# Kernel tuning notes

Hardware: AMD Instinct MI355X
Metric: run time of the kernel (lower is better)

Reference implementation:

```python
import jax, jax.numpy as jnp
import numpy as np

MAX_WAVELENGTH = 10000
BIG_NEG = -2.3819763e38

def _rope(x, positions):
    # x: [B, L, H, D], positions: [B, L] float32
    d = x.shape[-1]
    freq_exp = 2.0 / d * jnp.arange(d // 2, dtype=jnp.float32)
    timescale = MAX_WAVELENGTH ** freq_exp
    radians = (positions[..., None] / timescale[None, None, :])[..., None, :]  # [B,L,1,D/2]
    sin, cos = jnp.sin(radians), jnp.cos(radians)
    x1, x2 = jnp.split(x, 2, axis=-1)
    return jnp.concatenate([x1 * cos - x2 * sin, x2 * cos + x1 * sin], axis=-1).astype(x.dtype)

def _adaln_rmsnorm(x, cond, Wmod, bmod):
    # RMSNorm in fp32, then AdaLN scale/shift; returns (normed, gate[B,1,D])
    var = jnp.mean(jnp.square(x.astype(jnp.float32)), axis=-1, keepdims=True)
    normed = x * jax.lax.rsqrt(var + 1e-6)
    mod = (cond @ Wmod + bmod)[:, None, :]  # [B,1,3D]
    scale, shift, gate = jnp.split(mod, 3, axis=-1)
    return (normed * (1 + scale) + shift).astype(x.dtype), gate

def setup_inputs() -> dict:
    key = jax.random.key(0)
    ks = jax.random.split(key, 9)
    B, T, D, F, N, K, H = 2, 2048, 2048, 16384, 8, 1, 256
    x = jax.random.normal(ks[0], (B, T, D), jnp.float32)
    positions = jnp.broadcast_to(jnp.arange(T, dtype=jnp.float32), (B, T))
    attn_mask = jnp.broadcast_to(jnp.tril(jnp.ones((T, T), dtype=bool))[None, None], (B, 1, T, T))
    cond = jax.random.normal(ks[1], (B, D), jnp.float32)
    Wmod_a = jax.random.normal(ks[2], (D, 3 * D), jnp.float32) * 0.02
    bmod_a = jnp.zeros((3 * D,), jnp.float32)
    Wq = jax.random.normal(ks[3], (N, D, H), jnp.float32) * (D ** -0.5)
    Wkv = jax.random.normal(ks[4], (2, K, D, H), jnp.float32) * (D ** -0.5)
    Wo = jax.random.normal(ks[5], (N, H, D), jnp.float32) * ((N * H) ** -0.5)
    Wmod_f = jax.random.normal(ks[6], (D, 3 * D), jnp.float32) * 0.02
    bmod_f = jnp.zeros((3 * D,), jnp.float32)
    Wg = jax.random.normal(ks[7], (2, D, F), jnp.float32) * (D ** -0.5)
    Wl = jax.random.normal(ks[8], (F, D), jnp.float32) * (F ** -0.5)
    return dict(x=x, positions=positions, attn_mask=attn_mask, cond=cond,
                Wmod_a=Wmod_a, bmod_a=bmod_a, Wq=Wq, Wkv=Wkv, Wo=Wo,
                Wmod_f=Wmod_f, bmod_f=bmod_f, Wg=Wg, Wl=Wl)

def reference(x, positions, attn_mask, cond, Wmod_a, bmod_a, Wq, Wkv, Wo, Wmod_f, bmod_f, Wg, Wl):
    K = Wkv.shape[1]               # num_kv_heads
    H = Wq.shape[-1]               # head_dim
    # --- pre-attention AdaLN RMSNorm ---
    n, gate_a = _adaln_rmsnorm(x, cond, Wmod_a, bmod_a)
    # --- GQA projections ---
    q = jnp.einsum('BTD,NDH->BTNH', n, Wq)
    k = jnp.einsum('BSD,KDH->BSKH', n, Wkv[0])
    v = jnp.einsum('BSD,KDH->BSKH', n, Wkv[1])
    q = _rope(q, positions) * (H ** -0.5)
    k = _rope(k, positions)
    B, T, N, _ = q.shape
    q = q.reshape(B, T, K, N // K, H)  # B T K G H
    logits = jnp.einsum('BTKGH,BSKH->BKGTS', q, k, preferred_element_type=jnp.float32)
    masked = jnp.where(attn_mask[:, :, None, :, :], logits, BIG_NEG)
    probs = jax.nn.softmax(masked, axis=-1).astype(x.dtype)
    enc = jnp.einsum('BKGTS,BSKH->BTKGH', probs, v).reshape(B, T, N, H)
    attn_out = jnp.einsum('BTNH,NHD->BTD', enc, Wo)
    # gated residual
    x = x + attn_out * gate_a
    # --- pre-FFN AdaLN RMSNorm + gated-GeLU MLP ---
    n, gate_f = _adaln_rmsnorm(x, cond, Wmod_f, bmod_f)
    h = jax.nn.gelu(jnp.einsum('BTD,DF->BTF', n, Wg[0])) * jnp.einsum('BTD,DF->BTF', n, Wg[1])
    mlp_out = jnp.einsum('BTF,FD->BTD', h, Wl)
    return x + mlp_out * gate_f
```

## Files before the change

### kernel.cpp

```cpp
#include <hip/hip_runtime.h>
#include <hip/hip_bf16.h>

typedef __bf16 bf16_t;
typedef __bf16 bf16x8 __attribute__((ext_vector_type(8)));
typedef float  f32x4  __attribute__((ext_vector_type(4)));

#define DEV static __device__ __forceinline__

DEV void gload16(const bf16_t* g, bf16_t* l) {
    __builtin_amdgcn_global_load_lds(
        (const __attribute__((address_space(1))) void*)g,
        (__attribute__((address_space(3))) void*)l, 16, 0, 0);
}

enum { EPI_F32 = 0, EPI_BF16 = 1, EPI_RES = 2, EPI_GELU = 3, EPI_MUL = 4 };

#define MFMA16(QQ, AR, BR)                                                    \
  _Pragma("unroll")                                                           \
  for (int nj = 0; nj < 4; nj++) {                                            \
    acc[(QQ)*4+0][nj] = __builtin_amdgcn_mfma_f32_16x16x32_bf16(AR[0], BR[nj], acc[(QQ)*4+0][nj], 0, 0, 0); \
    acc[(QQ)*4+1][nj] = __builtin_amdgcn_mfma_f32_16x16x32_bf16(AR[1], BR[nj], acc[(QQ)*4+1][nj], 0, 0, 0); \
    acc[(QQ)*4+2][nj] = __builtin_amdgcn_mfma_f32_16x16x32_bf16(AR[2], BR[nj], acc[(QQ)*4+2][nj], 0, 0, 0); \
    acc[(QQ)*4+3][nj] = __builtin_amdgcn_mfma_f32_16x16x32_bf16(AR[3], BR[nj], acc[(QQ)*4+3][nj], 0, 0, 0); \
  }

#define READA(BUF, QQ, CI, AR)                                                \
  _Pragma("unroll")                                                           \
  for (int mi = 0; mi < 4; mi++)                                              \
    AR[mi] = *(const bf16x8*)(rbA##BUF##CI + (QQ) * 4096 + mi * 1024);

#define READB(BUF, CI, BR)                                                    \
  _Pragma("unroll")                                                           \
  for (int nj = 0; nj < 4; nj++)                                              \
    BR[nj] = *(const bf16x8*)(rbB##BUF##CI + nj * 1024);

#define PHASE(RD_STMT, QQ, AR, BR, STAGE_STMT, WAIT_STMT)                     \
  { RD_STMT STAGE_STMT                                                        \
    __builtin_amdgcn_s_barrier();                                             \
    asm volatile("s_waitcnt lgkmcnt(0)" ::: "memory");                        \
    __builtin_amdgcn_sched_barrier(0);                                        \
    __builtin_amdgcn_s_setprio(1);                                            \
    MFMA16(QQ, AR, BR);                                                       \
    __builtin_amdgcn_s_setprio(0);                                            \
    WAIT_STMT                                                                 \
    __builtin_amdgcn_s_barrier(); }

template<int EPI>
__global__ __launch_bounds__(512, 1)
void gemm8p(const bf16_t* __restrict__ A, const bf16_t* __restrict__ Bt,
            void* __restrict__ Cout, int Kd, int lda, int ldb, int ldc,
            long sCz,
            const float* __restrict__ res, const float* __restrict__ gate,
            int gateStride, int rowsPerB, const bf16_t* __restrict__ aux)
{
    const int nbx = gridDim.x;
    const int nwg = nbx * gridDim.y;
    int lin = blockIdx.y * nbx + blockIdx.x;
    const int q8 = nwg >> 3, r8 = nwg & 7;
    const int xcd = lin & 7, oo = lin >> 3;
    lin = (xcd < r8 ? xcd * (q8 + 1) : r8 * (q8 + 1) + (xcd - r8) * q8) + oo;
    const long m0 = (long)(lin / nbx) * 256;
    const long n0 = (long)(lin % nbx) * 256;
    const long kb = (long)blockIdx.z * Kd;

    const int tid = threadIdx.x;
    const int l   = tid & 63;
    const int w   = tid >> 6;
    const int wr  = w >> 2;
    const int wcn = w & 3;

    __shared__ bf16_t sA[2][16384];
    __shared__ bf16_t sB[2][16384];

    const long sgc = (long)(((l & 7) ^ (l >> 3)) << 3);
    const int NT = Kd >> 6;
    const int NI = NT >> 1;

    const bf16_t* pA0 = A + (m0 + 0 * 64 + w * 8 + (l >> 3)) * (long)lda + kb + sgc;
    const bf16_t* pA1 = A + (m0 + 1 * 64 + w * 8 + (l >> 3)) * (long)lda + kb + sgc;
    const bf16_t* pA2 = A + (m0 + 2 * 64 + w * 8 + (l >> 3)) * (long)lda + kb + sgc;
    const bf16_t* pA3 = A + (m0 + 3 * 64 + w * 8 + (l >> 3)) * (long)lda + kb + sgc;
    const bf16_t* pB0 = Bt + (n0 + 0 * 64 + w * 8 + (l >> 3)) * (long)ldb + kb + sgc;
    const bf16_t* pB1 = Bt + (n0 + 1 * 64 + w * 8 + (l >> 3)) * (long)ldb + kb + sgc;
    const bf16_t* pB2 = Bt + (n0 + 2 * 64 + w * 8 + (l >> 3)) * (long)ldb + kb + sgc;
    const bf16_t* pB3 = Bt + (n0 + 3 * 64 + w * 8 + (l >> 3)) * (long)ldb + kb + sgc;

#define SCA(kt, bi, c) gload16(pA##c + (kt), &sA[bi][(c) * 4096 + w * 512])
#define SCB(kt, bi, c) gload16(pB##c + (kt), &sB[bi][(c) * 4096 + w * 512])

    f32x4 acc[8][4];
#pragma unroll
    for (int i = 0; i < 8; i++)
#pragma unroll
        for (int j = 0; j < 4; j++) acc[i][j] = f32x4{0.f, 0.f, 0.f, 0.f};

    const int co0 = ((l >> 4) ^ (l & 7)) << 3;
    const int co1 = ((4 + (l >> 4)) ^ (l & 7)) << 3;

    const bf16_t* rbA00 = &sA[0][(wr * 128 + (l & 15)) * 64 + co0];
    const bf16_t* rbA01 = &sA[0][(wr * 128 + (l & 15)) * 64 + co1];
    const bf16_t* rbA10 = &sA[1][(wr * 128 + (l & 15)) * 64 + co0];
    const bf16_t* rbA11 = &sA[1][(wr * 128 + (l & 15)) * 64 + co1];
    const bf16_t* rbB00 = &sB[0][(wcn * 64 + (l & 15)) * 64 + co0];
    const bf16_t* rbB01 = &sB[0][(wcn * 64 + (l & 15)) * 64 + co1];
    const bf16_t* rbB10 = &sB[1][(wcn * 64 + (l & 15)) * 64 + co0];
    const bf16_t* rbB11 = &sB[1][(wcn * 64 + (l & 15)) * 64 + co1];

    SCA(0, 0, 0); SCA(0, 0, 1); SCA(0, 0, 2); SCA(0, 0, 3);
    SCB(0, 0, 0); SCB(0, 0, 1); SCB(0, 0, 2); SCB(0, 0, 3);
    SCA(64, 1, 0); SCA(64, 1, 2); SCB(64, 1, 0); SCB(64, 1, 1);
    asm volatile("s_waitcnt vmcnt(4)" ::: "memory");
    __builtin_amdgcn_s_barrier();

    bf16x8 b0[4], b1[4], aR[4];

    for (int it = 0; it < NI; ++it) {
        const long kv  = (long)(2 * it + 1) * 64;
        const long kc  = (long)(2 * it + 2) * 64;
        const long kd2 = (long)(2 * it + 3) * 64;
        const bool hc  = (2 * it + 2) < NT;

        PHASE({ READB(0, 0, b0); READA(0, 0, 0, aR); }, 0, aR, b0,
              { SCB(kv, 1, 2); SCB(kv, 1, 3); }, {})
        PHASE({ READB(0, 1, b1); READA(0, 0, 1, aR); }, 0, aR, b1,
              { SCA(kv, 1, 1); SCA(kv, 1, 3); }, {})
        PHASE({ READA(0, 1, 0, aR); }, 1, aR, b0,
              { if (hc) { SCA(kc, 0, 0); SCA(kc, 0, 2); } }, {})
        PHASE({ READA(0, 1, 1, aR); }, 1, aR, b1,
              { if (hc) { SCB(kc, 0, 0); SCB(kc, 0, 1); } },
              { if (hc) { asm volatile("s_waitcnt vmcnt(4)" ::: "memory"); }
                else    { asm volatile("s_waitcnt vmcnt(0)" ::: "memory"); } })
        PHASE({ READB(1, 0, b0); READA(1, 0, 0, aR); }, 0, aR, b0,
              { if (hc) { SCB(kc, 0, 2); SCB(kc, 0, 3); } }, {})
        PHASE({ READB(1, 1, b1); READA(1, 0, 1, aR); }, 0, aR, b1,
              { if (hc) { SCA(kc, 0, 1); SCA(kc, 0, 3); } }, {})
        PHASE({ READA(1, 1, 0, aR); }, 1, aR, b0,
              { if (hc) { SCA(kd2, 1, 0); SCA(kd2, 1, 2); } }, {})
        PHASE({ READA(1, 1, 1, aR); }, 1, aR, b1,
              { if (hc) { SCB(kd2, 1, 0); SCB(kd2, 1, 1); } },
              { if (hc) { asm volatile("s_waitcnt vmcnt(4)" ::: "memory"); }
                else    { asm volatile("s_waitcnt vmcnt(0)" ::: "memory"); } })
    }

#pragma unroll
    for (int mi = 0; mi < 8; mi++) {
#pragma unroll
        for (int nj = 0; nj < 4; nj++) {
            f32x4 v = acc[mi][nj];
            const long col   = n0 + wcn * 64 + nj * 16 + (l & 15);
            const long row0r = m0 + wr * 128 + mi * 16 + ((l >> 4) * 4);
#pragma unroll
            for (int e = 0; e < 4; e++) {
                const long row = row0r + e;
                const long idx = row * (long)ldc + col + (long)blockIdx.z * sCz;
                const float val = v[e];
                if constexpr (EPI == EPI_F32) {
                    ((float*)Cout)[idx] = val;
                } else if constexpr (EPI == EPI_BF16) {
                    ((bf16_t*)Cout)[idx] = (bf16_t)val;
                } else if constexpr (EPI == EPI_RES) {
                    const int b = (int)(row / rowsPerB);
                    ((float*)Cout)[idx] = res[row * (long)ldc + col] + val * gate[(long)b * gateStride + col];
                } else if constexpr (EPI == EPI_GELU) {
                    const float gl = 0.5f * val * (1.f + tanhf(0.7978845608f * (val + 0.044715f * val * val * val)));
                    ((bf16_t*)Cout)[idx] = (bf16_t)gl;
                } else if constexpr (EPI == EPI_MUL) {
                    ((bf16_t*)Cout)[idx] = (bf16_t)((float)aux[idx] * val);
                }
            }
        }
    }
#undef SCA
#undef SCB
}

__global__ __launch_bounds__(256)
void combine_splitk(const float* __restrict__ P, const float* __restrict__ X1,
                    const float* __restrict__ gate, float* __restrict__ out,
                    int D, int T, int gateStride, long zstride, long n4)
{
    for (long i4 = (long)blockIdx.x * 256 + threadIdx.x; i4 < n4; i4 += (long)gridDim.x * 256) {
        const long i = i4 * 4;
        const float4 p0 = *(const float4*)(P + i);
        const float4 p1 = *(const float4*)(P + i + zstride);
        const float4 xv = *(const float4*)(X1 + i);
        const long row = i / D;
        const int  b   = (int)(row / T);
        const int  col = (int)(i - row * D);
        const float* gp = gate + (long)b * gateStride + col;
        float4 r;
        r.x = xv.x + (p0.x + p1.x) * gp[0];
        r.y = xv.y + (p0.y + p1.y) * gp[1];
        r.z = xv.z + (p0.z + p1.z) * gp[2];
        r.w = xv.w + (p0.w + p1.w) * gp[3];
        *(float4*)(out + i) = r;
    }
}

template<int EPI, int CAUSAL>
__global__ __launch_bounds__(256)
void gemm_bt(const bf16_t* __restrict__ A, const bf16_t* __restrict__ Bt,
             void* __restrict__ Cout,
             int M, int N, int Kd, int lda, int ldb, int ldc,
             long sAz, long sBz, long sCz,
             const float* __restrict__ res, const float* __restrict__ gate,
             int gateStride, int rowsPerB, const bf16_t* __restrict__ aux)
{
    const int tid = threadIdx.x;
    const int l   = tid & 63;
    const int w   = tid >> 6;
    const int wr  = w >> 1, wc = w & 1;
    const long m0 = (long)blockIdx.y * 128;
    const long n0 = (long)blockIdx.x * 128;
    const int  z  = blockIdx.z;

    if constexpr (CAUSAL == 1) {
        if (n0 > m0 + 127) return;
    }
    int kend = Kd;
    if constexpr (CAUSAL == 2) {
        const int kc = (int)m0 + 128;
        kend = kc < Kd ? kc : Kd;
    }

    A  += (long)z * sAz;
    Bt += (long)z * sBz;

    __shared__ bf16_t As[128 * 32];
    __shared__ bf16_t Bs[128 * 32];

    const int srow = w * 16 + (l >> 2);
    const int scol = (l & 3) * 8;
    const bf16_t* Ag = A  + (m0 + srow) * (long)lda + scol;
    const bf16_t* Bg = Bt + (n0 + srow) * (long)ldb + scol;

    bf16_t* ldsA = As + w * 512;
    bf16_t* ldsB = Bs + w * 512;

    f32x4 acc[16];
    const f32x4 fz = {0.f, 0.f, 0.f, 0.f};
#pragma unroll
    for (int i = 0; i < 16; i++) acc[i] = fz;

    for (int k0 = 0; k0 < kend; k0 += 32) {
        gload16(Ag + k0,                  ldsA);
        gload16(Ag + k0 + 64 * (long)lda, ldsA + 2048);
        gload16(Bg + k0,                  ldsB);
        gload16(Bg + k0 + 64 * (long)ldb, ldsB + 2048);
        __syncthreads();

        bf16x8 af[4], bfr[4];
#pragma unroll
        for (int f = 0; f < 4; f++) {
            af[f]  = *(const bf16x8*)(As + (wr * 64 + f * 16 + (l & 15)) * 32 + (l >> 4) * 8);
            bfr[f] = *(const bf16x8*)(Bs + (wc * 64 + f * 16 + (l & 15)) * 32 + (l >> 4) * 8);
        }
#pragma unroll
        for (int i = 0; i < 4; i++)
#pragma unroll
            for (int j = 0; j < 4; j++)
                acc[i * 4 + j] = __builtin_amdgcn_mfma_f32_16x16x32_bf16(af[i], bfr[j], acc[i * 4 + j], 0, 0, 0);
        __syncthreads();
    }

#pragma unroll
    for (int i = 0; i < 4; i++) {
#pragma unroll
        for (int j = 0; j < 4; j++) {
            f32x4 v = acc[i * 4 + j];
            const long col  = n0 + wc * 64 + j * 16 + (l & 15);
            const long row0 = m0 + wr * 64 + i * 16 + ((l >> 4) * 4);
#pragma unroll
            for (int e = 0; e < 4; e++) {
                const long row = row0 + e;
                const long idx = row * (long)ldc + col + (long)z * sCz;
                const float val = v[e];
                if constexpr (EPI == EPI_F32) {
                    ((float*)Cout)[idx] = val;
                } else if constexpr (EPI == EPI_BF16) {
                    ((bf16_t*)Cout)[idx] = (bf16_t)val;
                } else if constexpr (EPI == EPI_RES) {
                    const int b = (int)(row / rowsPerB);
                    ((float*)Cout)[idx] = res[row * (long)ldc + col] + val * gate[(long)b * gateStride + col];
                } else if constexpr (EPI == EPI_GELU) {
                    const float gl = 0.5f * val * (1.f + tanhf(0.7978845608f * (val + 0.044715f * val * val * val)));
                    ((bf16_t*)Cout)[idx] = (bf16_t)gl;
                } else {
                    ((bf16_t*)Cout)[idx] = (bf16_t)((float)aux[idx] * val);
                }
            }
        }
    }
}

__global__ __launch_bounds__(256)
void transpose_f2b(const float* __restrict__ in, bf16_t* __restrict__ out,
                   int R, int C, long inStride, long outStride)
{
    __shared__ float tile[32][33];
    in  += (long)blockIdx.z * inStride;
    out += (long)blockIdx.z * outStride;
    const int c0 = blockIdx.x * 32, r0 = blockIdx.y * 32;
    const int tx = threadIdx.x, ty = threadIdx.y;
#pragma unroll
    for (int i = 0; i < 4; i++)
        tile[ty + i * 8][tx] = in[(long)(r0 + ty + i * 8) * C + c0 + tx];
    __syncthreads();
#pragma unroll
    for (int i = 0; i < 4; i++)
        out[(long)(c0 + ty + i * 8) * R + r0 + tx] = (bf16_t)tile[tx][ty + i * 8];
}

__global__ __launch_bounds__(256)
void modk_part(const float* __restrict__ cond, const float* __restrict__ W,
               float* __restrict__ part, int D3, int KS)
{
    const int j = blockIdx.x * 256 + threadIdx.x;
    const int b = blockIdx.y;
    const int z = blockIdx.z;
    const float* cb = cond + (long)b * (KS * gridDim.z);
    float s = 0.f;
    const int d0 = z * KS;
#pragma unroll 4
    for (int d = d0; d < d0 + KS; d++) s += cb[d] * W[(long)d * D3 + j];
    part[((long)z * gridDim.y + b) * D3 + j] = s;
}

__global__ __launch_bounds__(256)
void modk_reduce(const float* __restrict__ part, const float* __restrict__ bvec,
                 float* __restrict__ mod, int D3, int NZ)
{
    const int j = blockIdx.x * 256 + threadIdx.x;
    const int b = blockIdx.y;
    float s = bvec[j];
    for (int z = 0; z < NZ; z++) s += part[((long)z * gridDim.y + b) * D3 + j];
    mod[(long)b * D3 + j] = s;
}

__global__ __launch_bounds__(256)
void rmsnorm_adaln(const float* __restrict__ xin, const float* __restrict__ mod,
                   bf16_t* __restrict__ out, int D, int T, int D3)
{
    const long row = blockIdx.x;
    const int  b   = (int)(row / T);
    const int  tid = threadIdx.x;
    const float4* x4 = (const float4*)(xin + row * (long)D);
    const float4 v0 = x4[tid], v1 = x4[tid + 256];
    float ss = v0.x * v0.x + v0.y * v0.y + v0.z * v0.z + v0.w * v0.w
             + v1.x * v1.x + v1.y * v1.y + v1.z * v1.z + v1.w * v1.w;
    for (int o = 32; o; o >>= 1) ss += __shfl_down(ss, o, 64);
    __shared__ float red[4];
    if ((tid & 63) == 0) red[tid >> 6] = ss;
    __syncthreads();
    ss = red[0] + red[1] + red[2] + red[3];
    const float rs = rsqrtf(ss / (float)D + 1e-6f);
    const float* sc = mod + (long)b * D3;
    const float* sh = sc + D;
    const float4 s0 = ((const float4*)sc)[tid], s1 = ((const float4*)sc)[tid + 256];
    const float4 h0 = ((const float4*)sh)[tid], h1 = ((const float4*)sh)[tid + 256];
    bf16_t* orow = out + row * (long)D;
    orow[tid * 4 + 0]         = (bf16_t)(v0.x * rs * (1.f + s0.x) + h0.x);
    orow[tid * 4 + 1]         = (bf16_t)(v0.y * rs * (1.f + s0.y) + h0.y);
    orow[tid * 4 + 2]         = (bf16_t)(v0.z * rs * (1.f + s0.z) + h0.z);
    orow[tid * 4 + 3]         = (bf16_t)(v0.w * rs * (1.f + s0.w) + h0.w);
    orow[(tid + 256) * 4 + 0] = (bf16_t)(v1.x * rs * (1.f + s1.x) + h1.x);
    orow[(tid + 256) * 4 + 1] = (bf16_t)(v1.y * rs * (1.f + s1.y) + h1.y);
    orow[(tid + 256) * 4 + 2] = (bf16_t)(v1.z * rs * (1.f + s1.z) + h1.z);
    orow[(tid + 256) * 4 + 3] = (bf16_t)(v1.w * rs * (1.f + s1.w) + h1.w);
}

__global__ __launch_bounds__(128)
void rope_q(const bf16_t* __restrict__ qp, const float* __restrict__ positions,
            bf16_t* __restrict__ qo, int T, int ldq, int H)
{
    const int t = blockIdx.x, n = blockIdx.y, b = blockIdx.z;
    const int i = threadIdx.x;
    const long in0 = ((long)(b * T + t)) * ldq + n * H;
    const float x1 = (float)qp[in0 + i];
    const float x2 = (float)qp[in0 + i + 128];
    const float pos = positions[b * T + t];
    const float inv = expf(-9.210340371976184f * (float)i / 128.f);
    float s, c;
    sincosf(pos * inv, &s, &c);
    const float scl = 0.0625f;
    const long out0 = (((long)(b * 8 + n)) * T + t) * H;
    qo[out0 + i]       = (bf16_t)((x1 * c - x2 * s) * scl);
    qo[out0 + i + 128] = (bf16_t)((x2 * c + x1 * s) * scl);
}

__global__ __launch_bounds__(128)
void rope_kv(const bf16_t* __restrict__ kvp, const float* __restrict__ positions,
             bf16_t* __restrict__ ko, bf16_t* __restrict__ vt, int T, int H, int S, int ldkv)
{
    const int t = blockIdx.x, b = blockIdx.y;
    const int i = threadIdx.x;
    const long in0 = ((long)(b * T + t)) * ldkv;
    const float k1 = (float)kvp[in0 + i];
    const float k2 = (float)kvp[in0 + i + 128];
    const float pos = positions[b * T + t];
    const float inv = expf(-9.210340371976184f * (float)i / 128.f);
    float s, c;
    sincosf(pos * inv, &s, &c);
    const long ko0 = ((long)(b * T + t)) * H;
    ko[ko0 + i]       = (bf16_t)(k1 * c - k2 * s);
    ko[ko0 + i + 128] = (bf16_t)(k2 * c + k1 * s);
    vt[((long)b * H + i) * S + t]       = kvp[in0 + 256 + i];
    vt[((long)b * H + i + 128) * S + t] = kvp[in0 + 256 + i + 128];
}

__global__ __launch_bounds__(256)
void softmax_causal(const float* __restrict__ sc, bf16_t* __restrict__ pr, int T, int S)
{
    const int t = blockIdx.x, g = blockIdx.y;
    const long row = (long)g * T + t;
    const float* srow = sc + row * S;
    bf16_t* prow = pr + row * S;
    const int tid = threadIdx.x;
    const int limit = t | 127;
    const int nch = (limit >> 8) + 1;
    float vals[8];
    float mx = -3.4e38f;
    for (int i = 0; i < nch; i++) {
        const int s = i * 256 + tid;
        const float v = (s <= t) ? srow[s] : -3.4e38f;
        vals[i] = v;
        mx = fmaxf(mx, v);
    }
    for (int o = 32; o; o >>= 1) mx = fmaxf(mx, __shfl_down(mx, o, 64));
    __shared__ float red[4];
    if ((tid & 63) == 0) red[tid >> 6] = mx;
    __syncthreads();
    mx = fmaxf(fmaxf(red[0], red[1]), fmaxf(red[2], red[3]));
    __syncthreads();
    float sum = 0.f;
    for (int i = 0; i < nch; i++) {
        const int s = i * 256 + tid;
        const float e = (s <= t) ? __expf(vals[i] - mx) : 0.f;
        vals[i] = e;
        sum += e;
    }
    for (int o = 32; o; o >>= 1) sum += __shfl_down(sum, o, 64);
    if ((tid & 63) == 0) red[tid >> 6] = sum;
    __syncthreads();
    sum = red[0] + red[1] + red[2] + red[3];
    const float invs = 1.f / sum;
    for (int i = 0; i < nch; i++)
        prow[i * 256 + tid] = (bf16_t)(vals[i] * invs);
}

extern "C" void kernel_launch(void* const* d_in, const int* in_sizes, int n_in,
                              void* d_out, int out_size, void* d_ws, size_t ws_size,
                              hipStream_t stream)
{
    const float* x      = (const float*)d_in[0];
    const float* pos    = (const float*)d_in[1];
    const float* cond   = (const float*)d_in[3];
    const float* Wmod_a = (const float*)d_in[4];
    const float* bmod_a = (const float*)d_in[5];
    const float* Wq     = (const float*)d_in[6];
    const float* Wkv    = (const float*)d_in[7];
    const float* Wo     = (const float*)d_in[8];
    const float* Wmod_f = (const float*)d_in[9];
    const float* bmod_f = (const float*)d_in[10];
    const float* Wg     = (const float*)d_in[11];
    const float* Wl     = (const float*)d_in[12];

    constexpr int  Bb = 2, T = 2048, D = 2048, F = 16384, Nh = 8, H = 256;
    constexpr int  NH = 2048, S = 2048, G = 8, BT = 4096, D3 = 6144;
    constexpr int  KSLICE = 64, NZ = D / KSLICE;
    constexpr int  NQKV = 2560;

    char* ws = (char*)d_ws;
    size_t off = 0;
    auto alloc = [&](size_t bytes) { char* p = ws + off; off += bytes; return p; };

    bf16_t* WQT  = (bf16_t*)alloc((size_t)NH * D * 2);
    bf16_t* WKVT = (bf16_t*)alloc((size_t)512 * D * 2);
    bf16_t* WOT  = (bf16_t*)alloc((size_t)D * NH * 2);
    bf16_t* WGT  = (bf16_t*)alloc((size_t)2 * F * D * 2);
    bf16_t* WLT  = (bf16_t*)alloc((size_t)D * F * 2);
    float*  MODA = (float*)alloc((size_t)Bb * D3 * 4);
    float*  MODF = (float*)alloc((size_t)Bb * D3 * 4);
    float*  PART = (float*)alloc((size_t)NZ * Bb * D3 * 4);
    bf16_t* NA   = (bf16_t*)alloc((size_t)BT * D * 2);
    bf16_t* QKVP = (bf16_t*)alloc((size_t)BT * NQKV * 2);
    bf16_t* Qr   = (bf16_t*)alloc((size_t)Bb * Nh * T * H * 2);
    bf16_t* Kr   = (bf16_t*)alloc((size_t)Bb * T * H * 2);
    bf16_t* VT   = (bf16_t*)alloc((size_t)Bb * H * S * 2);
    bf16_t* ENC  = (bf16_t*)alloc((size_t)BT * NH * 2);
    float*  X1   = (float*)alloc((size_t)BT * D * 4);
    bf16_t* NF   = (bf16_t*)alloc((size_t)BT * D * 2);
    const size_t scBytes = (size_t)G * T * S * 4;
    const size_t prBytes = (size_t)G * T * S * 2;
    const size_t hBytes  = (size_t)BT * F * 2;
    const size_t bigBytes = (scBytes + prBytes > hBytes) ? (scBytes + prBytes) : hBytes;
    char* big = alloc(bigBytes);
    float*  SC = (float*)big;
    bf16_t* PR = (bf16_t*)(big + scBytes);
    bf16_t* Hb = (bf16_t*)big;
    float*  PARTK = (float*)(big + hBytes);
    (void)ws_size; (void)in_sizes; (void)n_in; (void)out_size;

    const dim3 tb(32, 8);
    transpose_f2b<<<dim3(H / 32, D / 32, 8), tb, 0, stream>>>(Wq,  WQT,  D,  H, (long)D * H, (long)H * D);
    transpose_f2b<<<dim3(H / 32, D / 32, 2), tb, 0, stream>>>(Wkv, WKVT, D,  H, (long)D * H, (long)H * D);
    transpose_f2b<<<dim3(D / 32, NH / 32, 1), tb, 0, stream>>>(Wo, WOT, NH,  D, 0, 0);
    transpose_f2b<<<dim3(F / 32, D / 32, 2), tb, 0, stream>>>(Wg,  WGT,  D,  F, (long)D * F, (long)F * D);
    transpose_f2b<<<dim3(D / 32, F / 32, 1), tb, 0, stream>>>(Wl,  WLT,  F,  D, 0, 0);
    modk_part<<<dim3(D3 / 256, Bb, NZ), 256, 0, stream>>>(cond, Wmod_a, PART, D3, KSLICE);
    modk_reduce<<<dim3(D3 / 256, Bb), 256, 0, stream>>>(PART, bmod_a, MODA, D3, NZ);
    modk_part<<<dim3(D3 / 256, Bb, NZ), 256, 0, stream>>>(cond, Wmod_f, PART, D3, KSLICE);
    modk_reduce<<<dim3(D3 / 256, Bb), 256, 0, stream>>>(PART, bmod_f, MODF, D3, NZ);
    rmsnorm_adaln<<<BT, 256, 0, stream>>>(x, MODA, NA, D, T, D3);
    gemm8p<EPI_BF16><<<dim3(NQKV / 256, BT / 256, 1), 512, 0, stream>>>(
        NA, WQT, QKVP, D, D, D, NQKV, 0, nullptr, nullptr, 0, 0, nullptr);
    rope_q<<<dim3(T, Nh, Bb), 128, 0, stream>>>(QKVP, pos, Qr, T, NQKV, H);
    rope_kv<<<dim3(T, Bb), 128, 0, stream>>>(QKVP + NH, pos, Kr, VT, T, H, S, NQKV);
    for (int b = 0; b < Bb; b++) {
        gemm_bt<EPI_F32, 1><<<dim3(S / 128, T / 128, G), 256, 0, stream>>>(
            Qr + (long)b * Nh * T * H, Kr + (long)b * T * H, SC,
            T, S, H, H, H, S, (long)T * H, 0, (long)T * S, nullptr, nullptr, 0, 0, nullptr);
        softmax_causal<<<dim3(T, G), 256, 0, stream>>>(SC, PR, T, S);
        gemm_bt<EPI_BF16, 2><<<dim3(H / 128, T / 128, G), 256, 0, stream>>>(
            PR, VT + (long)b * H * S, ENC + (long)b * T * NH,
            T, H, S, S, S, NH, (long)T * S, 0, (long)H, nullptr, nullptr, 0, 0, nullptr);
    }
    gemm8p<EPI_RES><<<dim3(D / 256, BT / 256, 1), 512, 0, stream>>>(
        ENC, WOT, X1, NH, NH, NH, D, 0, x, MODA + 2 * D, D3, T, nullptr);
    rmsnorm_adaln<<<BT, 256, 0, stream>>>(X1, MODF, NF, D, T, D3);
    gemm8p<EPI_GELU><<<dim3(F / 256, BT / 256, 1), 512, 0, stream>>>(
        NF, WGT, Hb, D, D, D, F, 0, nullptr, nullptr, 0, 0, nullptr);
    gemm8p<EPI_MUL><<<dim3(F / 256, BT / 256, 1), 512, 0, stream>>>(
        NF, WGT + (long)F * D, Hb, D, D, D, F, 0, nullptr, nullptr, 0, 0, Hb);
    gemm8p<EPI_F32><<<dim3(D / 256, BT / 256, 2), 512, 0, stream>>>(
        Hb, WLT, PARTK, F / 2, F, F, D, (long)BT * D, nullptr, nullptr, 0, 0, nullptr);
    combine_splitk<<<2048, 256, 0, stream>>>(
        PARTK, X1, MODF + 2 * D, (float*)d_out, D, T, D3, (long)BT * D, (long)BT * D / 4);
}
```

Before: 1.564 ms.

## Replace 8-phase ping-pong GEMM pipeline with simple double-buffered stage/compute loop

The main GEMM kernel drops its 8-phase interleaved schedule, which used split half-tile staging, setprio and sched barriers, in favour of a plainer double-buffered loop. Each iteration stages a full 64-wide K tile into the other buffer, waits, then runs all 32 MFMAs per sub-K chunk after loading 8 A and 4 B fragments at once. This cuts barrier count and scheduling complexity. It gives up the fine-grained overlap of LDS reads with MFMAs and the priority hints, and it raises register pressure from holding more fragments at once.

```diff
diff --git a/kernel.cpp b/kernel.cpp
--- a/kernel.cpp
+++ b/kernel.cpp
@@ -15,43 +15,37 @@
 
 enum { EPI_F32 = 0, EPI_BF16 = 1, EPI_RES = 2, EPI_GELU = 3, EPI_MUL = 4 };
 
-#define MFMA16(QQ, AR, BR)                                                    \
-  _Pragma("unroll")                                                           \
-  for (int nj = 0; nj < 4; nj++) {                                            \
-    acc[(QQ)*4+0][nj] = __builtin_amdgcn_mfma_f32_16x16x32_bf16(AR[0], BR[nj], acc[(QQ)*4+0][nj], 0, 0, 0); \
-    acc[(QQ)*4+1][nj] = __builtin_amdgcn_mfma_f32_16x16x32_bf16(AR[1], BR[nj], acc[(QQ)*4+1][nj], 0, 0, 0); \
-    acc[(QQ)*4+2][nj] = __builtin_amdgcn_mfma_f32_16x16x32_bf16(AR[2], BR[nj], acc[(QQ)*4+2][nj], 0, 0, 0); \
-    acc[(QQ)*4+3][nj] = __builtin_amdgcn_mfma_f32_16x16x32_bf16(AR[3], BR[nj], acc[(QQ)*4+3][nj], 0, 0, 0); \
+#define G_MFMA(d, a, b) d = __builtin_amdgcn_mfma_f32_16x16x32_bf16(a, b, d, 0, 0, 0)
+
+#define COMPUTE(AB0, AB1, BB0, BB1)                                           \
+  { bf16x8 aF[8], bF[4];                                                      \
+    _Pragma("unroll") for (int m8 = 0; m8 < 8; m8++)                          \
+      aF[m8] = *(const bf16x8*)(AB0 + (m8 >> 2) * 4096 + (m8 & 3) * 1024);    \
+    _Pragma("unroll") for (int nj = 0; nj < 4; nj++)                          \
+      bF[nj] = *(const bf16x8*)(BB0 + nj * 1024);                             \
+    _Pragma("unroll") for (int m8 = 0; m8 < 8; m8++)                          \
+      _Pragma("unroll") for (int nj = 0; nj < 4; nj++)                        \
+        G_MFMA(acc[m8][nj], aF[m8], bF[nj]);                                  \
+    _Pragma("unroll") for (int m8 = 0; m8 < 8; m8++)                          \
+      aF[m8] = *(const bf16x8*)(AB1 + (m8 >> 2) * 4096 + (m8 & 3) * 1024);    \
+    _Pragma("unroll") for (int nj = 0; nj < 4; nj++)                          \
+      bF[nj] = *(const bf16x8*)(BB1 + nj * 1024);                             \
+    _Pragma("unroll") for (int m8 = 0; m8 < 8; m8++)                          \
+      _Pragma("unroll") for (int nj = 0; nj < 4; nj++)                        \
+        G_MFMA(acc[m8][nj], aF[m8], bF[nj]);                                  \
   }
 
-#define READA(BUF, QQ, CI, AR)                                                \
-  _Pragma("unroll")                                                           \
-  for (int mi = 0; mi < 4; mi++)                                              \
-    AR[mi] = *(const bf16x8*)(rbA##BUF##CI + (QQ) * 4096 + mi * 1024);
-
-#define READB(BUF, CI, BR)                                                    \
-  _Pragma("unroll")                                                           \
-  for (int nj = 0; nj < 4; nj++)                                              \
-    BR[nj] = *(const bf16x8*)(rbB##BUF##CI + nj * 1024);
-
-#define PHASE(RD_STMT, QQ, AR, BR, STAGE_STMT, WAIT_STMT)                     \
-  { RD_STMT STAGE_STMT                                                        \
-    __builtin_amdgcn_s_barrier();                                             \
-    asm volatile("s_waitcnt lgkmcnt(0)" ::: "memory");                        \
-    __builtin_amdgcn_sched_barrier(0);                                        \
-    __builtin_amdgcn_s_setprio(1);                                            \
-    MFMA16(QQ, AR, BR);                                                       \
-    __builtin_amdgcn_s_setprio(0);                                            \
-    WAIT_STMT                                                                 \
-    __builtin_amdgcn_s_barrier(); }
+#define STAGE8(kt, bi)                                                        \
+  { SCA(kt, bi, 0); SCA(kt, bi, 1); SCA(kt, bi, 2); SCA(kt, bi, 3);           \
+    SCB(kt, bi, 0); SCB(kt, bi, 1); SCB(kt, bi, 2); SCB(kt, bi, 3); }
 
 template<int EPI>
 __global__ __launch_bounds__(512, 1)
-void gemm8p(const bf16_t* __restrict__ A, const bf16_t* __restrict__ Bt,
-            void* __restrict__ Cout, int Kd, int lda, int ldb, int ldc,
-            long sCz,
-            const float* __restrict__ res, const float* __restrict__ gate,
-            int gateStride, int rowsPerB, const bf16_t* __restrict__ aux)
+void gemma(const bf16_t* __restrict__ A, const bf16_t* __restrict__ Bt,
+           void* __restrict__ Cout, int Kd, int lda, int ldb, int ldc,
+           long sCz,
+           const float* __restrict__ res, const float* __restrict__ gate,
+           int gateStride, int rowsPerB, const bf16_t* __restrict__ aux)
 {
     const int nbx = gridDim.x;
     const int nwg = nbx * gridDim.y;
@@ -106,54 +100,40 @@
     const bf16_t* rbB10 = &sB[1][(wcn * 64 + (l & 15)) * 64 + co0];
     const bf16_t* rbB11 = &sB[1][(wcn * 64 + (l & 15)) * 64 + co1];
 
-    SCA(0, 0, 0); SCA(0, 0, 1); SCA(0, 0, 2); SCA(0, 0, 3);
-    SCB(0, 0, 0); SCB(0, 0, 1); SCB(0, 0, 2); SCB(0, 0, 3);
-    SCA(64, 1, 0); SCA(64, 1, 2); SCB(64, 1, 0); SCB(64, 1, 1);
-    asm volatile("s_waitcnt vmcnt(4)" ::: "memory");
-    __builtin_amdgcn_s_barrier();
-
-    bf16x8 b0[4], b1[4], aR[4];
+    STAGE8(0, 0);
 
     for (int it = 0; it < NI; ++it) {
-        const long kv  = (long)(2 * it + 1) * 64;
-        const long kc  = (long)(2 * it + 2) * 64;
-        const long kd2 = (long)(2 * it + 3) * 64;
-        const bool hc  = (2 * it + 2) < NT;
-
-        PHASE({ READB(0, 0, b0); READA(0, 0, 0, aR); }, 0, aR, b0,
-              { SCB(kv, 1, 2); SCB(kv, 1, 3); }, {})
-        PHASE({ READB(0, 1, b1); READA(0, 0, 1, aR); }, 0, aR, b1,
-              { SCA(kv, 1, 1); SCA(kv, 1, 3); }, {})
-        PHASE({ READA(0, 1, 0, aR); }, 1, aR, b0,
-              { if (hc) { SCA(kc, 0, 0); SCA(kc, 0, 2); } }, {})
-        PHASE({ READA(0, 1, 1, aR); }, 1, aR, b1,
-              { if (hc) { SCB(kc, 0, 0); SCB(kc, 0, 1); } },
-              { if (hc) { asm volatile("s_waitcnt vmcnt(4)" ::: "memory"); }
-                else    { asm volatile("s_waitcnt vmcnt(0)" ::: "memory"); } })
-        PHASE({ READB(1, 0, b0); READA(1, 0, 0, aR); }, 0, aR, b0,
-              { if (hc) { SCB(kc, 0, 2); SCB(kc, 0, 3); } }, {})
-        PHASE({ READB(1, 1, b1); READA(1, 0, 1, aR); }, 0, aR, b1,
-              { if (hc) { SCA(kc, 0, 1); SCA(kc, 0, 3); } }, {})
-        PHASE({ READA(1, 1, 0, aR); }, 1, aR, b0,
-              { if (hc) { SCA(kd2, 1, 0); SCA(kd2, 1, 2); } }, {})
-        PHASE({ READA(1, 1, 1, aR); }, 1, aR, b1,
-              { if (hc) { SCB(kd2, 1, 0); SCB(kd2, 1, 1); } },
-              { if (hc) { asm volatile("s_waitcnt vmcnt(4)" ::: "memory"); }
-                else    { asm volatile("s_waitcnt vmcnt(0)" ::: "memory"); } })
+        const int u = 2 * it, v = 2 * it + 1;
+        asm volatile("s_waitcnt lgkmcnt(0)" ::: "memory");
+        __builtin_amdgcn_s_barrier();
+        STAGE8((long)v * 64, 1);
+        asm volatile("s_waitcnt vmcnt(8)" ::: "memory");
+        __builtin_amdgcn_s_barrier();
+        COMPUTE(rbA00, rbA01, rbB00, rbB01);
+        asm volatile("s_waitcnt lgkmcnt(0)" ::: "memory");
+        __builtin_amdgcn_s_barrier();
+        if (v + 1 < NT) {
+            STAGE8((long)(v + 1) * 64, 0);
+            asm volatile("s_waitcnt vmcnt(8)" ::: "memory");
+        } else {
+            asm volatile("s_waitcnt vmcnt(0)" ::: "memory");
+        }
+        __builtin_amdgcn_s_barrier();
+        COMPUTE(rbA10, rbA11, rbB10, rbB11);
     }
 
 #pragma unroll
     for (int mi = 0; mi < 8; mi++) {
 #pragma unroll
         for (int nj = 0; nj < 4; nj++) {
-            f32x4 v = acc[mi][nj];
+            f32x4 vv = acc[mi][nj];
             const long col   = n0 + wcn * 64 + nj * 16 + (l & 15);
             const long row0r = m0 + wr * 128 + mi * 16 + ((l >> 4) * 4);
 #pragma unroll
             for (int e = 0; e < 4; e++) {
                 const long row = row0r + e;
                 const long idx = row * (long)ldc + col + (long)blockIdx.z * sCz;
-                const float val = v[e];
+                const float val = vv[e];
                 if constexpr (EPI == EPI_F32) {
                     ((float*)Cout)[idx] = val;
                 } else if constexpr (EPI == EPI_BF16) {
@@ -512,7 +492,7 @@
     modk_part<<<dim3(D3 / 256, Bb, NZ), 256, 0, stream>>>(cond, Wmod_f, PART, D3, KSLICE);
     modk_reduce<<<dim3(D3 / 256, Bb), 256, 0, stream>>>(PART, bmod_f, MODF, D3, NZ);
     rmsnorm_adaln<<<BT, 256, 0, stream>>>(x, MODA, NA, D, T, D3);
-    gemm8p<EPI_BF16><<<dim3(NQKV / 256, BT / 256, 1), 512, 0, stream>>>(
+    gemma<EPI_BF16><<<dim3(NQKV / 256, BT / 256, 1), 512, 0, stream>>>(
         NA, WQT, QKVP, D, D, D, NQKV, 0, nullptr, nullptr, 0, 0, nullptr);
     rope_q<<<dim3(T, Nh, Bb), 128, 0, stream>>>(QKVP, pos, Qr, T, NQKV, H);
     rope_kv<<<dim3(T, Bb), 128, 0, stream>>>(QKVP + NH, pos, Kr, VT, T, H, S, NQKV);
@@ -525,14 +505,14 @@
             PR, VT + (long)b * H * S, ENC + (long)b * T * NH,
             T, H, S, S, S, NH, (long)T * S, 0, (long)H, nullptr, nullptr, 0, 0, nullptr);
     }
-    gemm8p<EPI_RES><<<dim3(D / 256, BT / 256, 1), 512, 0, stream>>>(
+    gemma<EPI_RES><<<dim3(D / 256, BT / 256, 1), 512, 0, stream>>>(
         ENC, WOT, X1, NH, NH, NH, D, 0, x, MODA + 2 * D, D3, T, nullptr);
     rmsnorm_adaln<<<BT, 256, 0, stream>>>(X1, MODF, NF, D, T, D3);
-    gemm8p<EPI_GELU><<<dim3(F / 256, BT / 256, 1), 512, 0, stream>>>(
+    gemma<EPI_GELU><<<dim3(F / 256, BT / 256, 1), 512, 0, stream>>>(
         NF, WGT, Hb, D, D, D, F, 0, nullptr, nullptr, 0, 0, nullptr);
-    gemm8p<EPI_MUL><<<dim3(F / 256, BT / 256, 1), 512, 0, stream>>>(
+    gemma<EPI_MUL><<<dim3(F / 256, BT / 256, 1), 512, 0, stream>>>(
         NF, WGT + (long)F * D, Hb, D, D, D, F, 0, nullptr, nullptr, 0, 0, Hb);
-    gemm8p<EPI_F32><<<dim3(D / 256, BT / 256, 2), 512, 0, stream>>>(
+    gemma<EPI_F32><<<dim3(D / 256, BT / 256, 2), 512, 0, stream>>>(
         Hb, WLT, PARTK, F / 2, F, F, D, (long)BT * D, nullptr, nullptr, 0, 0, nullptr);
     combine_splitk<<<2048, 256, 0, stream>>>(
         PARTK, X1, MODF + 2 * D, (float*)d_out, D, T, D3, (long)BT * D, (long)BT * D / 4);
```

New measurement: 1.545 ms. No clear change (-1.2%).
